# Performance work log

Hardware: AMD Instinct MI355X
Metric: run time of the kernel (lower is better)

The kernel has to match this reference:

```python
import jax, jax.numpy as jnp
import numpy as np

D_IN = 1024
D_OUT = 1024
N, S = 4, 2048

def setup_inputs() -> dict:
    key = jax.random.key(0)
    kv, kk, kq, k1, k2, k3 = jax.random.split(key, 6)
    return {
        "v": jax.random.normal(kv, (N, S, D_IN), dtype=jnp.float32),
        "k": jax.random.normal(kk, (N, S, D_IN), dtype=jnp.float32),
        "q": jax.random.normal(kq, (N, S, D_IN), dtype=jnp.float32),
        "WV": jax.random.normal(k1, (D_OUT, D_IN), dtype=jnp.float32),
        "WQ": jax.random.normal(k2, (D_OUT, D_IN), dtype=jnp.float32),
        "WK": jax.random.normal(k3, (D_OUT, D_IN), dtype=jnp.float32),
    }

def reference(v, k, q, WV, WQ, WK) -> jnp.ndarray:
    # projections: x @ W.T  -> [N, S, D_OUT]
    wv = jnp.einsum('nsw,ow->nso', v, WV)
    wk = jnp.einsum('nsw,ow->nso', k, WK)
    wq = jnp.einsum('nsw,ow->nso', q, WQ)
    # scores [N, Sq, Sk]; NOTE: softmax over axis=1 (query axis, matching torch dim=1),
    # then post-hoc division by input_shape[0] AFTER softmax (faithful to source).
    scores = jnp.einsum('nqo,nko->nqk', wq, wk)
    wqk = jax.nn.softmax(scores, axis=1) / jnp.float32(D_IN)
    return jnp.einsum('nqk,nko->nqo', wqk, wv)
```

## Files before the change

### kernel.cpp

```cpp
#include <hip/hip_runtime.h>
#include <math.h>


typedef _Float16 f16;
typedef _Float16 f16x8 __attribute__((ext_vector_type(8)));
typedef _Float16 f16x4 __attribute__((ext_vector_type(4)));
typedef float f32x4 __attribute__((ext_vector_type(4)));

enum StageMode { SM_PLANES2, SM_PLANES1 };
enum EpiMode   { EPI_F32, EPI_SPLIT, EPI_F16T };

#define GLL_PITCH 32

__device__ __forceinline__ void gll16(const f16* g, f16* l) {
    __builtin_amdgcn_global_load_lds(
        (const __attribute__((address_space(1))) void*)g,
        (__attribute__((address_space(3))) void*)l, 16, 0, 0);
}

__device__ __forceinline__ void stage_gll_plane(const f16* __restrict__ gplane,
                                                f16* __restrict__ lds,
                                                long rowBase, int ld, int k0,
                                                int wave, int lane)
{
#pragma unroll
    for (int i = 0; i < 2; i++) {
        int slotBase = (wave * 2 + i) * 64;
        int t = slotBase + lane;
        int r = t >> 2;
        int c = (t & 3) ^ ((r >> 1) & 3);
        const f16* g = gplane + (rowBase + r) * (long)ld + k0 + c * 8;
        gll16(g, lds + (long)slotBase * 8);
    }
}

__device__ __forceinline__ int frag_off_gll(int row, int g) {
    return row * GLL_PITCH + ((g ^ ((row >> 1) & 3)) << 3);
}

template<StageMode SA, StageMode SB, EpiMode EP, int GROUPM, bool STATS>
__global__ __launch_bounds__(256, 4)
void mfma_gemm(const f16* __restrict__ Ahi, const f16* __restrict__ Alo,
               const f16* __restrict__ Bhi, const f16* __restrict__ Blo,
               float* __restrict__ pmOut, float* __restrict__ psOut,
               void* __restrict__ C0, void* __restrict__ C1,
               int M, int Nc, int K, int lda, int ldb, int ldc,
               long batchA, long batchB, long batchC,
               float epiScale, int tsShift)
{
    constexpr bool TRIPLE = (SA == SM_PLANES2);
    constexpr int PLANE_SZ = 128 * GLL_PITCH;

    int bx, by;
    if constexpr (GROUPM > 0) {
        int gx = gridDim.x;
        int lin = blockIdx.y * gx + blockIdx.x;
        int nig = GROUPM * gx;
        int gid = lin / nig;
        int rem = lin - gid * nig;
        by = gid * GROUPM + (rem % GROUPM);
        bx = rem / GROUPM;
    } else {
        bx = blockIdx.x;
        by = blockIdx.y;
    }
    const int n0 = bx * 128;
    const int m0 = by * 128;
    const long z = blockIdx.z;

    const long aOfs = z * batchA, bOfs = z * batchB, cOfs = z * batchC;

    __shared__ __align__(16) f16 As_hi[PLANE_SZ];
    __shared__ __align__(16) f16 Bs_hi[PLANE_SZ];
    __shared__ __align__(16) f16 As_lo[TRIPLE ? PLANE_SZ : 8];
    __shared__ __align__(16) f16 Bs_lo[TRIPLE ? PLANE_SZ : 8];

    const int tid  = threadIdx.x;
    const int lane = tid & 63;
    const int wave = tid >> 6;
    const int wr = (wave >> 1) * 64;
    const int wc = (wave & 1) * 64;
    const int fm = lane & 15;
    const int fg = lane >> 4;

    f32x4 acc[4][4];
#pragma unroll
    for (int i = 0; i < 4; i++)
#pragma unroll
        for (int j = 0; j < 4; j++) acc[i][j] = (f32x4){0.f, 0.f, 0.f, 0.f};

    int roA[4], roB[4];
#pragma unroll
    for (int i = 0; i < 4; i++) {
        roA[i] = frag_off_gll(wr + i * 16 + fm, fg);
        roB[i] = frag_off_gll(wc + i * 16 + fm, fg);
    }

    for (int k0 = 0; k0 < K; k0 += 32) {
        stage_gll_plane(Ahi + aOfs, As_hi, m0, lda, k0, wave, lane);
        stage_gll_plane(Bhi + bOfs, Bs_hi, n0, ldb, k0, wave, lane);
        if constexpr (TRIPLE) {
            stage_gll_plane(Alo + aOfs, As_lo, m0, lda, k0, wave, lane);
            stage_gll_plane(Blo + bOfs, Bs_lo, n0, ldb, k0, wave, lane);
        }
        __syncthreads();

        f16x8 ah[4], bh[4], al[4], bl[4];
#pragma unroll
        for (int i = 0; i < 4; i++) {
            ah[i] = *(const f16x8*)&As_hi[roA[i]];
            bh[i] = *(const f16x8*)&Bs_hi[roB[i]];
            if constexpr (TRIPLE) {
                al[i] = *(const f16x8*)&As_lo[roA[i]];
                bl[i] = *(const f16x8*)&Bs_lo[roB[i]];
            }
        }
#pragma unroll
        for (int i = 0; i < 4; i++) {
#pragma unroll
            for (int j = 0; j < 4; j++) {
                acc[i][j] = __builtin_amdgcn_mfma_f32_16x16x32_f16(ah[i], bh[j], acc[i][j], 0, 0, 0);
                if constexpr (TRIPLE) {
                    acc[i][j] = __builtin_amdgcn_mfma_f32_16x16x32_f16(ah[i], bl[j], acc[i][j], 0, 0, 0);
                    acc[i][j] = __builtin_amdgcn_mfma_f32_16x16x32_f16(al[i], bh[j], acc[i][j], 0, 0, 0);
                }
            }
        }
        __syncthreads();
    }

    const int cr = fg * 4;
    const int cn = fm;
#pragma unroll
    for (int i = 0; i < 4; i++) {
#pragma unroll
        for (int j = 0; j < 4; j++) {
#pragma unroll
            for (int r = 0; r < 4; r++) {
                long mg = m0 + wr + i * 16 + cr + r;
                long ng = n0 + wc + j * 16 + cn;
                float val = acc[i][j][r] * epiScale;
                if constexpr (EP == EPI_F32) {
                    ((float*)C0)[cOfs + mg * ldc + ng] = val;
                } else if constexpr (EP == EPI_SPLIT) {
                    f16 h = (f16)val;
                    ((f16*)C0)[cOfs + mg * ldc + ng] = h;
                    ((f16*)C1)[cOfs + mg * ldc + ng] = (f16)(val - (float)h);
                } else {
                    long TS = 1L << tsShift;
                    long nb = mg >> tsShift;
                    long s  = mg & (TS - 1);
                    long addr = nb * ((long)Nc << tsShift) + ng * TS + s;
                    ((f16*)C0)[addr] = (f16)val;
                }
            }
        }
    }

    if constexpr (STATS) {
        __shared__ float stM[2][128];
        __shared__ float stS[2][128];
#pragma unroll
        for (int j = 0; j < 4; j++) {
            float mj = -3.402823466e38f;
#pragma unroll
            for (int i = 0; i < 4; i++)
#pragma unroll
                for (int r = 0; r < 4; r++) mj = fmaxf(mj, acc[i][j][r]);
            float sj = 0.f;
#pragma unroll
            for (int i = 0; i < 4; i++)
#pragma unroll
                for (int r = 0; r < 4; r++) sj += __expf(acc[i][j][r] - mj);
#pragma unroll
            for (int mask = 16; mask <= 32; mask <<= 1) {
                float mo = __shfl_xor(mj, mask, 64);
                float so = __shfl_xor(sj, mask, 64);
                float mn = fmaxf(mj, mo);
                sj = sj * __expf(mj - mn) + so * __expf(mo - mn);
                mj = mn;
            }
            if (fg == 0) {
                stM[wave >> 1][wc + j * 16 + cn] = mj;
                stS[wave >> 1][wc + j * 16 + cn] = sj;
            }
        }
        __syncthreads();
        if (tid < 128) {
            float ma = stM[0][tid], mb = stM[1][tid];
            float Mc = fmaxf(ma, mb);
            float Sv = stS[0][tid] * __expf(ma - Mc) + stS[1][tid] * __expf(mb - Mc);
            long o = ((long)z * (M >> 7) + by) * (long)Nc + (long)bx * 128 + tid;
            pmOut[o] = Mc;
            psOut[o] = Sv;
        }
    }
}

template<bool HAS_LO>
__global__ __launch_bounds__(256)
void split_kernel(const float* __restrict__ src, f16* __restrict__ hi,
                  f16* __restrict__ lo, long n)
{
    long i = ((long)blockIdx.x * 256 + threadIdx.x) * 8;
    if (i >= n) return;
    float4 x0 = *(const float4*)&src[i];
    float4 x1 = *(const float4*)&src[i + 4];
    float xs[8] = {x0.x, x0.y, x0.z, x0.w, x1.x, x1.y, x1.z, x1.w};
    f16x8 h, l;
#pragma unroll
    for (int e = 0; e < 8; e++) {
        f16 hh = (f16)xs[e];
        h[e] = hh;
        if (HAS_LO) l[e] = (f16)(xs[e] - (float)hh);
    }
    *(f16x8*)&hi[i] = h;
    if (HAS_LO) *(f16x8*)&lo[i] = l;
}

__global__ __launch_bounds__(64)
void stats_combine_kernel(const float* __restrict__ pm, const float* __restrict__ ps,
                          float* __restrict__ statM, float* __restrict__ statR, int S)
{
    const int n = blockIdx.y;
    const int kk = blockIdx.x * 64 + threadIdx.x;
    float M = -INFINITY;
#pragma unroll
    for (int i = 0; i < 16; i++)
        M = fmaxf(M, pm[((long)n * 16 + i) * S + kk]);
    float Ssum = 0.f;
#pragma unroll
    for (int i = 0; i < 16; i++)
        Ssum += ps[((long)n * 16 + i) * S + kk] * __expf(pm[((long)n * 16 + i) * S + kk] - M);
    statM[(long)n * S + kk] = M;
    statR[(long)n * S + kk] = 1.0f / Ssum;
}

__global__ __launch_bounds__(256)
void pmat_kernel(const float* __restrict__ Sc, const float* __restrict__ statM,
                 const float* __restrict__ statR, f16* __restrict__ Phi, int S)
{
    const int n = blockIdx.z;
    const int kk = blockIdx.x * 1024 + threadIdx.x * 4;
    const float* Sn = Sc + (long)n * S * S;
    f16* ph = Phi + (long)n * S * S;
    float4 M4 = *(const float4*)&statM[(long)n * S + kk];
    float4 R4 = *(const float4*)&statR[(long)n * S + kk];
    const int q0 = blockIdx.y * 32;
    for (int qi = 0; qi < 32; qi++) {
        long idx = (long)(q0 + qi) * S + kk;
        float4 x = *(const float4*)&Sn[idx];
        f16x4 p;
        p[0] = (f16)(__expf(x.x - M4.x) * R4.x);
        p[1] = (f16)(__expf(x.y - M4.y) * R4.y);
        p[2] = (f16)(__expf(x.z - M4.z) * R4.z);
        p[3] = (f16)(__expf(x.w - M4.w) * R4.w);
        *(f16x4*)&ph[idx] = p;
    }
}

extern "C" void kernel_launch(void* const* d_in, const int* in_sizes, int n_in,
                              void* d_out, int out_size, void* d_ws, size_t ws_size,
                              hipStream_t stream)
{
    const float* v  = (const float*)d_in[0];
    const float* k  = (const float*)d_in[1];
    const float* q  = (const float*)d_in[2];
    const float* WV = (const float*)d_in[3];
    const float* WQ = (const float*)d_in[4];
    const float* WK = (const float*)d_in[5];
    float* out = (float*)d_out;

    const int N = 4, S = 2048, D = 1024;
    const long NSD = (long)N * S * D;
    const long DD  = (long)D * D;

    f16* ws = (f16*)d_ws;
    f16* q_hi = ws;
    f16* q_lo = ws + NSD;
    f16* k_hi = ws + 2 * NSD;
    f16* k_lo = ws + 3 * NSD;
    f16* v_hi = ws + 4 * NSD;
    f16* Wb   = ws + 5 * NSD;
    f16* WQ_hi = Wb,          *WQ_lo = Wb + DD;
    f16* WK_hi = Wb + 2 * DD, *WK_lo = Wb + 3 * DD;
    f16* WV_hi = Wb + 4 * DD;
    f16* wq_hi = ws + 5 * NSD + 5 * DD;
    f16* wq_lo = wq_hi + NSD;
    f16* wk_hi = wq_hi + 2 * NSD;
    f16* wk_lo = wq_hi + 3 * NSD;
    f16* wvT_hi = ws;
    float* Sc   = (float*)(ws + NSD);
    f16* P_hi   = wq_hi;
    float* pm    = (float*)(ws + 9 * NSD + 5 * DD);
    float* ps    = pm + (long)N * 16 * S;
    float* statM = ps + (long)N * 16 * S;
    float* statR = statM + (long)N * S;

    dim3 blk(256);

    split_kernel<true ><<<dim3(NSD / 2048), blk, 0, stream>>>(q,  q_hi, q_lo, NSD);
    split_kernel<true ><<<dim3(NSD / 2048), blk, 0, stream>>>(k,  k_hi, k_lo, NSD);
    split_kernel<false><<<dim3(NSD / 2048), blk, 0, stream>>>(v,  v_hi, nullptr, NSD);
    split_kernel<true ><<<dim3(DD / 2048),  blk, 0, stream>>>(WQ, WQ_hi, WQ_lo, DD);
    split_kernel<true ><<<dim3(DD / 2048),  blk, 0, stream>>>(WK, WK_hi, WK_lo, DD);
    split_kernel<false><<<dim3(DD / 2048),  blk, 0, stream>>>(WV, WV_hi, nullptr, DD);

    {
        dim3 g(D / 128, (N * S) / 128, 1);
        mfma_gemm<SM_PLANES2, SM_PLANES2, EPI_SPLIT, 4, false><<<g, blk, 0, stream>>>(
            q_hi, q_lo, WQ_hi, WQ_lo, nullptr, nullptr, wq_hi, wq_lo,
            N * S, D, D, D, D, D, 0, 0, 0, 1.0f, 0);
        mfma_gemm<SM_PLANES2, SM_PLANES2, EPI_SPLIT, 4, false><<<g, blk, 0, stream>>>(
            k_hi, k_lo, WK_hi, WK_lo, nullptr, nullptr, wk_hi, wk_lo,
            N * S, D, D, D, D, D, 0, 0, 0, 1.0f, 0);
        mfma_gemm<SM_PLANES1, SM_PLANES1, EPI_F16T, 4, false><<<g, blk, 0, stream>>>(
            v_hi, nullptr, WV_hi, nullptr, nullptr, nullptr, wvT_hi, nullptr,
            N * S, D, D, D, D, 0, 0, 0, 0, 1.0f, 11 );
    }
    {
        dim3 g(S / 128, S / 128, N);
        mfma_gemm<SM_PLANES2, SM_PLANES2, EPI_F32, 4, true><<<g, blk, 0, stream>>>(
            wq_hi, wq_lo, wk_hi, wk_lo, pm, ps, Sc, nullptr,
            S, S, D, D, D, S, (long)S * D, (long)S * D, (long)S * S, 1.0f, 0);
    }
    {
        dim3 gB(S / 64, N);
        stats_combine_kernel<<<gB, dim3(64), 0, stream>>>(pm, ps, statM, statR, S);
    }
    {
        dim3 g(S / 1024, S / 32, N);
        pmat_kernel<<<g, blk, 0, stream>>>(Sc, statM, statR, P_hi, S);
    }
    {
        dim3 g(D / 128, S / 128, N);
        mfma_gemm<SM_PLANES1, SM_PLANES1, EPI_F32, 4, false><<<g, blk, 0, stream>>>(
            P_hi, nullptr, wvT_hi, nullptr, nullptr, nullptr, out, nullptr,
            S, D, S, S, S, D, (long)S * S, (long)S * D, (long)S * D, 1.0f / (float)D, 0);
    }
}
```

Measured before the change: 471.8 us.

## Add dedicated 256x256-tile scores GEMM with 512 threads and fused stats

Replaces the generic 128x128 split-precision GEMM for the Q·K^T scores with a specialized kernel. It uses 256x256 tiles, 8 waves, double-buffered global-to-LDS loads and s_setprio around the MFMA bursts. The larger tile raises operand reuse per LDS load and cuts the number of per-column partial max/sum chunks from 16 to 8, so the stats combine kernel is templated on the chunk count. In exchange it uses about 128KB of LDS and many accumulator registers per block, which limits occupancy to one block per CU. The grid becomes 256 blocks.

Result: no change. 472.8 us (+0.2%).

```diff
diff --git a/kernel.cpp b/kernel.cpp
--- a/kernel.cpp
+++ b/kernel.cpp
@@ -197,6 +197,167 @@
     }
 }
 
+__global__ __launch_bounds__(512, 2)
+void scores_gemm(const f16* __restrict__ Ahi, const f16* __restrict__ Alo,
+                 const f16* __restrict__ Bhi, const f16* __restrict__ Blo,
+                 float* __restrict__ pmOut, float* __restrict__ psOut,
+                 float* __restrict__ C,
+                 int M, int Nc, int K, int lda, int ldb, int ldc,
+                 long batchA, long batchB, long batchC)
+{
+    constexpr int PLANE = 256 * GLL_PITCH;
+
+    __shared__ __align__(16) f16 As_hi[2][PLANE];
+    __shared__ __align__(16) f16 As_lo[2][PLANE];
+    __shared__ __align__(16) f16 Bs_hi[2][PLANE];
+    __shared__ __align__(16) f16 Bs_lo[2][PLANE];
+
+    const int tid  = threadIdx.x;
+    const int lane = tid & 63;
+    const int wave = tid >> 6;
+    const int rw   = wave >> 2;
+    const int cw   = wave & 3;
+    const int wrM  = rw * 128;
+    const int wrN  = cw * 64;
+    const int fm   = lane & 15;
+    const int fg   = lane >> 4;
+
+    const int n0 = blockIdx.x * 256;
+    const int m0 = blockIdx.y * 256;
+    const long z = blockIdx.z;
+    const long aOfs = z * batchA, bOfs = z * batchB, cOfs = z * batchC;
+
+    int slotBase[2], srcA[2], srcB[2];
+#pragma unroll
+    for (int i = 0; i < 2; i++) {
+        int sb = (wave * 2 + i) * 64;
+        int t  = sb + lane;
+        int r  = t >> 2;
+        int c  = (t & 3) ^ ((r >> 1) & 3);
+        slotBase[i] = sb * 8;
+        srcA[i] = (m0 + r) * lda + c * 8;
+        srcB[i] = (n0 + r) * ldb + c * 8;
+    }
+
+#define SC_STAGE(buf, k0) do {                                              \
+    _Pragma("unroll")                                                        \
+    for (int s_ = 0; s_ < 2; s_++) {                                         \
+        gll16(Ahi + aOfs + srcA[s_] + (k0), &As_hi[buf][slotBase[s_]]);      \
+        gll16(Alo + aOfs + srcA[s_] + (k0), &As_lo[buf][slotBase[s_]]);      \
+        gll16(Bhi + bOfs + srcB[s_] + (k0), &Bs_hi[buf][slotBase[s_]]);      \
+        gll16(Blo + bOfs + srcB[s_] + (k0), &Bs_lo[buf][slotBase[s_]]);      \
+    } } while (0)
+
+    f32x4 acc[8][4];
+#pragma unroll
+    for (int i = 0; i < 8; i++)
+#pragma unroll
+        for (int j = 0; j < 4; j++) acc[i][j] = (f32x4){0.f, 0.f, 0.f, 0.f};
+
+    int roA[8], roB[4];
+#pragma unroll
+    for (int i = 0; i < 8; i++) roA[i] = frag_off_gll(wrM + i * 16 + fm, fg);
+#pragma unroll
+    for (int j = 0; j < 4; j++) roB[j] = frag_off_gll(wrN + j * 16 + fm, fg);
+
+    const int NT = K >> 5;
+    SC_STAGE(0, 0);
+
+    for (int t = 0; t < NT; t++) {
+        const int cur = t & 1;
+        __syncthreads();
+        if (t + 1 < NT) SC_STAGE(cur ^ 1, (t + 1) * 32);
+
+        f16x8 bh[4], bl[4];
+#pragma unroll
+        for (int j = 0; j < 4; j++) {
+            bh[j] = *(const f16x8*)&Bs_hi[cur][roB[j]];
+            bl[j] = *(const f16x8*)&Bs_lo[cur][roB[j]];
+        }
+#pragma unroll
+        for (int h = 0; h < 2; h++) {
+            f16x8 ah[4], al[4];
+#pragma unroll
+            for (int i = 0; i < 4; i++) {
+                ah[i] = *(const f16x8*)&As_hi[cur][roA[h * 4 + i]];
+                al[i] = *(const f16x8*)&As_lo[cur][roA[h * 4 + i]];
+            }
+            __builtin_amdgcn_s_setprio(1);
+#pragma unroll
+            for (int i = 0; i < 4; i++)
+#pragma unroll
+                for (int j = 0; j < 4; j++)
+                    acc[h * 4 + i][j] = __builtin_amdgcn_mfma_f32_16x16x32_f16(
+                        ah[i], bh[j], acc[h * 4 + i][j], 0, 0, 0);
+#pragma unroll
+            for (int i = 0; i < 4; i++)
+#pragma unroll
+                for (int j = 0; j < 4; j++)
+                    acc[h * 4 + i][j] = __builtin_amdgcn_mfma_f32_16x16x32_f16(
+                        ah[i], bl[j], acc[h * 4 + i][j], 0, 0, 0);
+#pragma unroll
+            for (int i = 0; i < 4; i++)
+#pragma unroll
+                for (int j = 0; j < 4; j++)
+                    acc[h * 4 + i][j] = __builtin_amdgcn_mfma_f32_16x16x32_f16(
+                        al[i], bh[j], acc[h * 4 + i][j], 0, 0, 0);
+            __builtin_amdgcn_s_setprio(0);
+        }
+    }
+#undef SC_STAGE
+
+    const int cr = fg * 4;
+#pragma unroll
+    for (int i = 0; i < 8; i++) {
+#pragma unroll
+        for (int j = 0; j < 4; j++) {
+#pragma unroll
+            for (int r = 0; r < 4; r++) {
+                long mg = m0 + wrM + i * 16 + cr + r;
+                long ng = n0 + wrN + j * 16 + fm;
+                C[cOfs + mg * (long)ldc + ng] = acc[i][j][r];
+            }
+        }
+    }
+
+    __shared__ float stM[2][256];
+    __shared__ float stS[2][256];
+#pragma unroll
+    for (int j = 0; j < 4; j++) {
+        float mj = -3.402823466e38f;
+#pragma unroll
+        for (int i = 0; i < 8; i++)
+#pragma unroll
+            for (int r = 0; r < 4; r++) mj = fmaxf(mj, acc[i][j][r]);
+        float sj = 0.f;
+#pragma unroll
+        for (int i = 0; i < 8; i++)
+#pragma unroll
+            for (int r = 0; r < 4; r++) sj += __expf(acc[i][j][r] - mj);
+#pragma unroll
+        for (int mask = 16; mask <= 32; mask <<= 1) {
+            float mo = __shfl_xor(mj, mask, 64);
+            float so = __shfl_xor(sj, mask, 64);
+            float mn = fmaxf(mj, mo);
+            sj = sj * __expf(mj - mn) + so * __expf(mo - mn);
+            mj = mn;
+        }
+        if (fg == 0) {
+            stM[rw][wrN + j * 16 + fm] = mj;
+            stS[rw][wrN + j * 16 + fm] = sj;
+        }
+    }
+    __syncthreads();
+    if (tid < 256) {
+        float ma = stM[0][tid], mb = stM[1][tid];
+        float Mc = fmaxf(ma, mb);
+        float Sv = stS[0][tid] * __expf(ma - Mc) + stS[1][tid] * __expf(mb - Mc);
+        long o = ((long)z * (M >> 8) + blockIdx.y) * (long)Nc + (long)blockIdx.x * 256 + tid;
+        pmOut[o] = Mc;
+        psOut[o] = Sv;
+    }
+}
+
 template<bool HAS_LO>
 __global__ __launch_bounds__(256)
 void split_kernel(const float* __restrict__ src, f16* __restrict__ hi,
@@ -218,6 +379,7 @@
     if (HAS_LO) *(f16x8*)&lo[i] = l;
 }
 
+template<int CH>
 __global__ __launch_bounds__(64)
 void stats_combine_kernel(const float* __restrict__ pm, const float* __restrict__ ps,
                           float* __restrict__ statM, float* __restrict__ statR, int S)
@@ -226,12 +388,12 @@
     const int kk = blockIdx.x * 64 + threadIdx.x;
     float M = -INFINITY;
 #pragma unroll
-    for (int i = 0; i < 16; i++)
-        M = fmaxf(M, pm[((long)n * 16 + i) * S + kk]);
+    for (int i = 0; i < CH; i++)
+        M = fmaxf(M, pm[((long)n * CH + i) * S + kk]);
     float Ssum = 0.f;
 #pragma unroll
-    for (int i = 0; i < 16; i++)
-        Ssum += ps[((long)n * 16 + i) * S + kk] * __expf(pm[((long)n * 16 + i) * S + kk] - M);
+    for (int i = 0; i < CH; i++)
+        Ssum += ps[((long)n * CH + i) * S + kk] * __expf(pm[((long)n * CH + i) * S + kk] - M);
     statM[(long)n * S + kk] = M;
     statR[(long)n * S + kk] = 1.0f / Ssum;
 }
@@ -293,8 +455,8 @@
     float* Sc   = (float*)(ws + NSD);
     f16* P_hi   = wq_hi;
     float* pm    = (float*)(ws + 9 * NSD + 5 * DD);
-    float* ps    = pm + (long)N * 16 * S;
-    float* statM = ps + (long)N * 16 * S;
+    float* ps    = pm + (long)N * 8 * S;
+    float* statM = ps + (long)N * 8 * S;
     float* statR = statM + (long)N * S;
 
     dim3 blk(256);
@@ -319,14 +481,14 @@
             N * S, D, D, D, D, 0, 0, 0, 0, 1.0f, 11 );
     }
     {
-        dim3 g(S / 128, S / 128, N);
-        mfma_gemm<SM_PLANES2, SM_PLANES2, EPI_F32, 4, true><<<g, blk, 0, stream>>>(
-            wq_hi, wq_lo, wk_hi, wk_lo, pm, ps, Sc, nullptr,
-            S, S, D, D, D, S, (long)S * D, (long)S * D, (long)S * S, 1.0f, 0);
+        dim3 g(S / 256, S / 256, N);
+        scores_gemm<<<g, dim3(512), 0, stream>>>(
+            wq_hi, wq_lo, wk_hi, wk_lo, pm, ps, Sc,
+            S, S, D, D, D, S, (long)S * D, (long)S * D, (long)S * S);
     }
     {
         dim3 gB(S / 64, N);
-        stats_combine_kernel<<<gB, dim3(64), 0, stream>>>(pm, ps, statM, statR, S);
+        stats_combine_kernel<8><<<gB, dim3(64), 0, stream>>>(pm, ps, statM, statR, S);
     }
     {
         dim3 g(S / 1024, S / 32, N);
```
